# Optimization experiments

Measured on AMD Instinct MI355X. Metric: run time of the kernel, lower is better.

Reference implementation:

```python
import jax, jax.numpy as jnp
import numpy as np
from jax import lax

D_MODEL = 1024
D_STATE = 16
D_CONV = 4
EXPAND = 2
D_INNER = EXPAND * D_MODEL
DT_RANK = (D_MODEL + 15) // 16  # ceil(d_model/16) = 64


def setup_inputs() -> dict:
    key = jax.random.key(0)
    ks = jax.random.split(key, 10)
    B, L = 4, 2048
    hidden_states = jax.random.normal(ks[0], (B, L, D_MODEL), dtype=jnp.float32)
    # parameters
    in_proj_w = jax.random.normal(ks[1], (2 * D_INNER, D_MODEL), dtype=jnp.float32) / np.sqrt(D_MODEL)
    conv_w = jax.random.normal(ks[2], (D_INNER, D_CONV), dtype=jnp.float32) / np.sqrt(D_CONV)
    conv_b = jax.random.normal(ks[3], (D_INNER,), dtype=jnp.float32) * 0.02
    x_proj_w = jax.random.normal(ks[4], (DT_RANK + 2 * D_STATE, D_INNER), dtype=jnp.float32) / np.sqrt(D_INNER)
    dt_init_std = DT_RANK ** -0.5
    dt_proj_w = jax.random.uniform(ks[5], (D_INNER, DT_RANK), minval=-dt_init_std, maxval=dt_init_std, dtype=jnp.float32)
    # dt bias: inverse-softplus of log-uniform dt in [dt_min, dt_max]
    dt_min, dt_max = 1e-3, 1e-1
    dt = jnp.exp(jax.random.uniform(ks[6], (D_INNER,)) * (np.log(dt_max) - np.log(dt_min)) + np.log(dt_min))
    dt = jnp.clip(dt, 1e-4)
    dt_proj_b = dt + jnp.log(-jnp.expm1(-dt))
    A_log = jnp.log(jnp.broadcast_to(jnp.arange(1, D_STATE + 1, dtype=jnp.float32), (D_INNER, D_STATE)))
    D = jnp.ones((D_INNER,), dtype=jnp.float32)
    out_proj_w = jax.random.normal(ks[7], (D_MODEL, D_INNER), dtype=jnp.float32) / np.sqrt(D_INNER)
    return {"hidden_states": hidden_states, "in_proj_w": in_proj_w, "conv_w": conv_w,
            "conv_b": conv_b, "x_proj_w": x_proj_w, "dt_proj_w": dt_proj_w,
            "dt_proj_b": dt_proj_b, "A_log": A_log, "D": D, "out_proj_w": out_proj_w}


def reference(hidden_states, in_proj_w, conv_w, conv_b, x_proj_w, dt_proj_w, dt_proj_b, A_log, D, out_proj_w):
    Bb, L, _ = hidden_states.shape
    # input projection -> x, z each (B, L, d_inner)
    xz = jnp.einsum('bld,ed->ble', hidden_states, in_proj_w)
    x, z = jnp.split(xz, 2, axis=-1)
    # depthwise causal conv1d over time, then SiLU
    x_c = jnp.transpose(x, (0, 2, 1))  # (B, Di, L)
    x_c = lax.conv_general_dilated(x_c, conv_w[:, None, :], window_strides=(1,),
                                   padding=[(D_CONV - 1, 0)], feature_group_count=D_INNER,
                                   dimension_numbers=('NCH', 'OIH', 'NCH'))
    x_act = jax.nn.silu(x_c + conv_b[:, None])            # (B, Di, L)
    u = jnp.transpose(x_act, (0, 2, 1))                   # (B, L, Di)
    # time-variant dt, B, C projections
    x_dbl = jnp.einsum('bld,ed->ble', u, x_proj_w)        # (B, L, R+2N)
    dt_lo = x_dbl[..., :DT_RANK]
    Bm = x_dbl[..., DT_RANK:DT_RANK + D_STATE]            # (B, L, N)
    Cm = x_dbl[..., DT_RANK + D_STATE:]                   # (B, L, N)
    delta = jax.nn.softplus(jnp.einsum('blr,dr->bld', dt_lo, dt_proj_w) + dt_proj_b)  # (B, L, Di)
    A = -jnp.exp(A_log)                                   # (Di, N)

    def step(h, inp):
        d_t, b_t, c_t, u_t = inp                          # (B,Di),(B,N),(B,N),(B,Di)
        dA = jnp.exp(d_t[:, :, None] * A)                 # (B, Di, N)
        h = h * dA + (d_t * u_t)[:, :, None] * b_t[:, None, :]
        y_t = jnp.einsum('bdn,bn->bd', h, c_t)
        return h, y_t

    h0 = jnp.zeros((Bb, D_INNER, D_STATE), dtype=jnp.float32)
    xs = (jnp.swapaxes(delta, 0, 1), jnp.swapaxes(Bm, 0, 1), jnp.swapaxes(Cm, 0, 1), jnp.swapaxes(u, 0, 1))
    _, ys = lax.scan(step, h0, xs)                        # (L, B, Di)
    y = jnp.swapaxes(ys, 0, 1) + D * u                    # skip connection D*u
    y = y * jax.nn.silu(z)                                # gating
    return jnp.einsum('bld,od->blo', y, out_proj_w)
```

## Files before the change

### kernel.cpp

```cpp
#include <hip/hip_runtime.h>
#include <cmath>

#define BATCH   4
#define SEQLEN  2048
#define NTOK    (BATCH*SEQLEN)
#define DMODEL  1024
#define DINNER  2048
#define DSTATE  16
#define DTRANK  64
#define NCHUNK  32
#define LCHUNK  64

typedef unsigned short u16;
typedef __attribute__((ext_vector_type(8))) short          bf16x8;
typedef __attribute__((ext_vector_type(8))) unsigned short u16x8;
typedef __attribute__((ext_vector_type(4))) float          f32x4;

__device__ __forceinline__ float sigmoid_precise(float x){ return 1.f/(1.f+expf(-x)); }
__device__ __forceinline__ float b2f(u16 h){ return __uint_as_float(((unsigned)h)<<16); }
__device__ __forceinline__ u16 f2b(float x){
    unsigned u = __float_as_uint(x);
    u += 0x7fffu + ((u>>16)&1u);
    return (u16)(u>>16);
}
__device__ __forceinline__ ushort4 pack4(float a,float b,float c,float d){
    ushort4 r; r.x=f2b(a); r.y=f2b(b); r.z=f2b(c); r.w=f2b(d); return r;
}

__device__ __forceinline__ void gld_lds16(const void* g, void* l){
    __builtin_amdgcn_global_load_lds(
        (const __attribute__((address_space(1))) void*)g,
        (__attribute__((address_space(3))) void*)l,
        16, 0, 0);
}

__device__ __forceinline__ void decay_powers(float e1, float* dec){
    float e2=e1*e1, e3=e2*e1, e4=e2*e2;
    float e5=e4*e1, e6=e4*e2, e7=e4*e3, e8=e4*e4;
    dec[0]=e1; dec[1]=e2; dec[2]=e3; dec[3]=e4;
    dec[4]=e5; dec[5]=e6; dec[6]=e7; dec[7]=e8;
    dec[8]=e8*e1; dec[9]=e8*e2; dec[10]=e8*e3; dec[11]=e8*e4;
    dec[12]=e8*e5; dec[13]=e8*e6; dec[14]=e8*e7; dec[15]=e8*e8;
}

#define CVT_N0 (NTOK*DMODEL/8)
#define CVT_N1 (2*DINNER*DMODEL/8)
#define CVT_N2 (DMODEL*DINNER/8)
#define CVT_N3 (96*DINNER/8)
#define CVT_N4 (DINNER*DTRANK/8)
#define CVT_TOT (CVT_N0+CVT_N1+CVT_N2+CVT_N3+CVT_N4)

__global__ __launch_bounds__(256)
void cvt_all(const float* __restrict__ s0, const float* __restrict__ s1,
             const float* __restrict__ s2, const float* __restrict__ s3,
             const float* __restrict__ s4, u16* __restrict__ dst)
{
    int i = blockIdx.x*256 + threadIdx.x;
    if (i >= CVT_TOT) return;
    const float* s; int off = i;
    if      (off <  CVT_N0){ s = s0; }
    else if ((off -= CVT_N0) < CVT_N1){ s = s1; }
    else if ((off -= CVT_N1) < CVT_N2){ s = s2; }
    else if ((off -= CVT_N2) < CVT_N3){ s = s3; }
    else    { off -= CVT_N3; s = s4; }
    const float4* sp = (const float4*)(s + (size_t)off*8);
    float4 a = sp[0], b = sp[1];
    *(ushort4*)(dst + (size_t)i*8)     = pack4(a.x,a.y,a.z,a.w);
    *(ushort4*)(dst + (size_t)i*8 + 4) = pack4(b.x,b.y,b.z,b.w);
}

__global__ __launch_bounds__(512, 1)
void gemm_xz8(const u16* __restrict__ A, const u16* __restrict__ B,
              u16* __restrict__ Cx, u16* __restrict__ Cz)
{
    __shared__ u16 lds[2][2][256*64];
    const int tid  = threadIdx.x;
    const int lane = tid & 63;
    const int wave = tid >> 6;
    const int wm = wave >> 2, wn = wave & 3;
    const int fr = lane & 15, quad = lane >> 4;
    const int bid = blockIdx.x;
    const int swz = (bid & 7) * 64 + (bid >> 3);
    const int m0 = (swz >> 4) * 256;
    const int n0 = (swz & 15) * 256;
    const int NT = DMODEL / 64;

    const int srow  = tid >> 3;
    const int colsw = (((tid & 7) ^ (srow & 7)) << 3);
    const u16* gA = A + (size_t)(m0 + srow)*DMODEL + colsw;
    const u16* gB = B + (size_t)(n0 + srow)*DMODEL + colsw;

#define STAGE_A(t,h) do{ \
    const u16* g_ = gA + (size_t)((h)*128)*DMODEL + (t)*64; \
    u16* l_ = &lds[(t)&1][0][(h)*8192 + tid*8]; \
    gld_lds16(g_, l_); gld_lds16(g_ + (size_t)64*DMODEL, l_ + 4096); }while(0)
#define STAGE_B(t,h) do{ \
    const u16* g_ = gB + (size_t)((h)*128)*DMODEL + (t)*64; \
    u16* l_ = &lds[(t)&1][1][(h)*8192 + tid*8]; \
    gld_lds16(g_, l_); gld_lds16(g_ + (size_t)64*DMODEL, l_ + 4096); }while(0)

    const int cs0 = ((quad    ) ^ (fr & 7)) << 3;
    const int cs1 = ((quad + 4) ^ (fr & 7)) << 3;
    const int aoff = (wm*128 + fr) * 64;
    const int boff = (wn*64  + fr) * 64;

    f32x4 acc[8][4];
#pragma unroll
    for (int m=0;m<8;m++)
#pragma unroll
        for (int n=0;n<4;n++)
#pragma unroll
            for (int e=0;e<4;e++) acc[m][n][e] = 0.f;

    STAGE_A(0,0); STAGE_A(0,1); STAGE_B(0,0); STAGE_B(0,1);
    STAGE_B(1,0); STAGE_B(1,1);
    asm volatile("s_waitcnt vmcnt(4)" ::: "memory");
    __builtin_amdgcn_s_barrier();
    __builtin_amdgcn_sched_barrier(0);

#define XZ_MFMA_PAIR(MB) \
    _Pragma("unroll") \
    for (int n=0;n<4;n++){ \
        acc[MB][n]   = __builtin_amdgcn_mfma_f32_16x16x32_bf16(aP0, bF[n][0], acc[MB][n],   0,0,0); \
        acc[MB][n]   = __builtin_amdgcn_mfma_f32_16x16x32_bf16(aP1, bF[n][1], acc[MB][n],   0,0,0); \
        acc[MB+1][n] = __builtin_amdgcn_mfma_f32_16x16x32_bf16(aQ0, bF[n][0], acc[MB+1][n], 0,0,0); \
        acc[MB+1][n] = __builtin_amdgcn_mfma_f32_16x16x32_bf16(aQ1, bF[n][1], acc[MB+1][n], 0,0,0); \
    }

    for (int t=0; t<NT; ++t){
        const u16* lA = &lds[t&1][0][0];
        const u16* lB = &lds[t&1][1][0];
        bf16x8 bF[4][2];

        {
            bf16x8 aP0 = *(const bf16x8*)&lA[aoff + 0*1024 + cs0];
            bf16x8 aP1 = *(const bf16x8*)&lA[aoff + 0*1024 + cs1];
            bf16x8 aQ0 = *(const bf16x8*)&lA[aoff + 1*1024 + cs0];
            bf16x8 aQ1 = *(const bf16x8*)&lA[aoff + 1*1024 + cs1];
#pragma unroll
            for (int n=0;n<4;n++){
                bF[n][0] = *(const bf16x8*)&lB[boff + n*1024 + cs0];
                bF[n][1] = *(const bf16x8*)&lB[boff + n*1024 + cs1];
            }
            if (t+1 < NT) STAGE_A(t+1,0);
            asm volatile("s_waitcnt lgkmcnt(8)" ::: "memory");
            __builtin_amdgcn_s_barrier();
            asm volatile("s_waitcnt lgkmcnt(0)" ::: "memory");
            __builtin_amdgcn_s_setprio(1);
            XZ_MFMA_PAIR(0)
            __builtin_amdgcn_s_setprio(0);
            __builtin_amdgcn_s_barrier();
            __builtin_amdgcn_sched_barrier(0);
        }
        {
            bf16x8 aP0 = *(const bf16x8*)&lA[aoff + 2*1024 + cs0];
            bf16x8 aP1 = *(const bf16x8*)&lA[aoff + 2*1024 + cs1];
            bf16x8 aQ0 = *(const bf16x8*)&lA[aoff + 3*1024 + cs0];
            bf16x8 aQ1 = *(const bf16x8*)&lA[aoff + 3*1024 + cs1];
            if (t+2 < NT) STAGE_B(t+2,0);
            __builtin_amdgcn_s_barrier();
            asm volatile("s_waitcnt lgkmcnt(0)" ::: "memory");
            __builtin_amdgcn_s_setprio(1);
            XZ_MFMA_PAIR(2)
            __builtin_amdgcn_s_setprio(0);
            __builtin_amdgcn_s_barrier();
            __builtin_amdgcn_sched_barrier(0);
        }
        {
            bf16x8 aP0 = *(const bf16x8*)&lA[aoff + 4*1024 + cs0];
            bf16x8 aP1 = *(const bf16x8*)&lA[aoff + 4*1024 + cs1];
            bf16x8 aQ0 = *(const bf16x8*)&lA[aoff + 5*1024 + cs0];
            bf16x8 aQ1 = *(const bf16x8*)&lA[aoff + 5*1024 + cs1];
            if (t+1 < NT) STAGE_A(t+1,1);
            __builtin_amdgcn_s_barrier();
            asm volatile("s_waitcnt lgkmcnt(0)" ::: "memory");
            __builtin_amdgcn_s_setprio(1);
            XZ_MFMA_PAIR(4)
            __builtin_amdgcn_s_setprio(0);
            __builtin_amdgcn_s_barrier();
            __builtin_amdgcn_sched_barrier(0);
        }
        {
            bf16x8 aP0 = *(const bf16x8*)&lA[aoff + 6*1024 + cs0];
            bf16x8 aP1 = *(const bf16x8*)&lA[aoff + 6*1024 + cs1];
            bf16x8 aQ0 = *(const bf16x8*)&lA[aoff + 7*1024 + cs0];
            bf16x8 aQ1 = *(const bf16x8*)&lA[aoff + 7*1024 + cs1];
            if (t+2 < NT) STAGE_B(t+2,1);
            __builtin_amdgcn_s_barrier();
            asm volatile("s_waitcnt lgkmcnt(0)" ::: "memory");
            __builtin_amdgcn_s_setprio(1);
            XZ_MFMA_PAIR(6)
            __builtin_amdgcn_s_setprio(0);
            if (t < NT-2) asm volatile("s_waitcnt vmcnt(2)" ::: "memory");
            else          asm volatile("s_waitcnt vmcnt(0)" ::: "memory");
            __builtin_amdgcn_s_barrier();
            __builtin_amdgcn_sched_barrier(0);
        }
    }
#undef XZ_MFMA_PAIR
#undef STAGE_A
#undef STAGE_B

    const bool is_z = (n0 >= DINNER);
    u16* dst = is_z ? Cz : Cx;
    const int nb = (is_z ? n0 - DINNER : n0) + wn*64;
#pragma unroll
    for (int m=0;m<8;m++){
        const int rbase = m0 + wm*128 + m*16 + quad*4;
#pragma unroll
        for (int reg=0;reg<4;reg++){
            const int row = rbase + reg;
#pragma unroll
            for (int n=0;n<4;n++){
                float x = acc[m][n][reg];
                if (is_z) x = x * sigmoid_precise(x);
                dst[(size_t)row*DINNER + nb + n*16 + fr] = f2b(x);
            }
        }
    }
}

template<int EPI>
__global__ __launch_bounds__(256, 4)
void gemm_bt(const u16* __restrict__ A, int lda,
             const u16* __restrict__ B, int ldb,
             void* __restrict__ Cx, void* __restrict__ Cz, int ldc,
             int K)
{
    __shared__ u16 As[128*32];
    __shared__ u16 Bs[128*32];
    const int tid  = threadIdx.x;
    const int lane = tid & 63, wave = tid >> 6;
    const int wm = (wave & 1) * 64, wn = (wave >> 1) * 64;
    const int fr = lane & 15, quad = lane >> 4;
    const int m0 = blockIdx.y * 128;
    const int n0 = blockIdx.x * 128;

    f32x4 acc[4][4];
#pragma unroll
    for (int i=0;i<4;i++)
#pragma unroll
        for (int j=0;j<4;j++)
#pragma unroll
            for (int e=0;e<4;e++) acc[i][j][e] = 0.f;

    for (int k0=0;k0<K;k0+=32){
#pragma unroll
        for (int r=0;r<2;r++){
            int i = tid + 256*r;
            gld_lds16(&A[(size_t)(m0 + (i>>2))*lda + k0 + (i&3)*8], &As[(size_t)i*8]);
        }
#pragma unroll
        for (int r=0;r<2;r++){
            int i = tid + 256*r;
            gld_lds16(&B[(size_t)(n0 + (i>>2))*ldb + k0 + (i&3)*8], &Bs[(size_t)i*8]);
        }
        __syncthreads();

        bf16x8 af[4], bfg[4];
#pragma unroll
        for (int i=0;i<4;i++) af[i]  = *(const bf16x8*)&As[(wm + i*16 + fr)*32 + quad*8];
#pragma unroll
        for (int j=0;j<4;j++) bfg[j] = *(const bf16x8*)&Bs[(wn + j*16 + fr)*32 + quad*8];
#pragma unroll
        for (int i=0;i<4;i++)
#pragma unroll
            for (int j=0;j<4;j++)
                acc[i][j] = __builtin_amdgcn_mfma_f32_16x16x32_bf16(af[i], bfg[j], acc[i][j], 0,0,0);
        __syncthreads();
    }

    if (EPI==0){
        float* C = (float*)Cx;
#pragma unroll
        for (int i=0;i<4;i++){
            int rbase = m0 + wm + i*16 + quad*4;
#pragma unroll
            for (int reg=0;reg<4;reg++){
                int row = rbase + reg;
#pragma unroll
                for (int j=0;j<4;j++)
                    C[(size_t)row*ldc + n0 + wn + j*16 + fr] = acc[i][j][reg];
            }
        }
    } else {
        const bool is_z = (n0 >= DINNER);
        u16* dst = is_z ? (u16*)Cz : (u16*)Cx;
        const int nb = is_z ? (n0 - DINNER) : n0;
#pragma unroll
        for (int i=0;i<4;i++){
            int rbase = m0 + wm + i*16 + quad*4;
#pragma unroll
            for (int reg=0;reg<4;reg++){
                int row = rbase + reg;
#pragma unroll
                for (int j=0;j<4;j++){
                    float x = acc[i][j][reg];
                    if (is_z) x = x * sigmoid_precise(x);
                    dst[(size_t)row*ldc + nb + wn + j*16 + fr] = f2b(x);
                }
            }
        }
    }
}

__global__ __launch_bounds__(256)
void conv_silu_sw(const u16* __restrict__ xb, const float* __restrict__ conv_w,
                  const float* __restrict__ conv_b, u16* __restrict__ ub)
{
    const int d0 = (blockIdx.x*256 + threadIdx.x)*4;
    const int bl = blockIdx.y;
    const int b  = bl >> 6, lc = bl & 63;
    const int l0 = lc*32;
    float4 w[4]; float bias[4];
#pragma unroll
    for (int j=0;j<4;j++){ w[j] = *(const float4*)&conv_w[(d0+j)*4]; bias[j] = conv_b[d0+j]; }

    const size_t base = (size_t)b*SEQLEN*DINNER + d0;
    float win[4][3];
#pragma unroll
    for (int j=0;j<4;j++) win[j][0]=win[j][1]=win[j][2]=0.f;
    if (l0 > 0){
#pragma unroll
        for (int t=0;t<3;t++){
            ushort4 v = *(const ushort4*)&xb[base + (size_t)(l0-3+t)*DINNER];
            win[0][t]=b2f(v.x); win[1][t]=b2f(v.y); win[2][t]=b2f(v.z); win[3][t]=b2f(v.w);
        }
    }
    for (int l=l0; l<l0+32; l++){
        ushort4 v = *(const ushort4*)&xb[base + (size_t)l*DINNER];
        float x3[4] = {b2f(v.x), b2f(v.y), b2f(v.z), b2f(v.w)};
        ushort4 o;
        u16* op = (u16*)&o;
#pragma unroll
        for (int j=0;j<4;j++){
            float acc = bias[j];
            acc = fmaf(w[j].x, win[j][0], acc);
            acc = fmaf(w[j].y, win[j][1], acc);
            acc = fmaf(w[j].z, win[j][2], acc);
            acc = fmaf(w[j].w, x3[j],     acc);
            op[j] = f2b(acc * sigmoid_precise(acc));
            win[j][0]=win[j][1]; win[j][1]=win[j][2]; win[j][2]=x3[j];
        }
        *(ushort4*)&ub[base + (size_t)l*DINNER] = o;
    }
}

__global__ __launch_bounds__(256, 4)
void gemm_xproj_mfma(const u16* __restrict__ u, const u16* __restrict__ W,
                     u16* __restrict__ dtlo, float* __restrict__ bc)
{
    __shared__ u16 As[3][32*64];
    __shared__ u16 Bs[3][96*64];
    const int tid  = threadIdx.x;
    const int lane = tid & 63, wave = tid >> 6;
    const int fr = lane & 15, quad = lane >> 4;
    const int mi = wave & 1, nh = wave >> 1;
    const int m0 = blockIdx.x * 32;
    const int NT = DINNER/64;

    const int arow = (tid & 127) >> 2;
    const u16* pA = u + (size_t)(m0 + arow)*DINNER + (tid>>7)*32 + (tid&3)*8;
    const u16* pB[3];
#pragma unroll
    for (int r=0;r<3;r++){
        int i = tid + 256*r;
        int ks = (i >= 384) ? 1 : 0;
        int rem = i - ks*384;
        pB[r] = W + (size_t)(rem>>2)*DINNER + ks*32 + (rem&3)*8;
    }

#pragma unroll
    for (int t=0; t<2; ++t){
        gld_lds16(pA + t*64, &As[t][tid*8]);
#pragma unroll
        for (int r=0;r<3;r++)
            gld_lds16(pB[r] + t*64, &Bs[t][(tid + 256*r)*8]);
    }

    f32x4 acc[3];
#pragma unroll
    for (int j=0;j<3;j++)
#pragma unroll
        for (int e=0;e<4;e++) acc[j][e] = 0.f;

    int s = 0;
    for (int t=0; t<NT; ++t){
        if (t < NT-1) asm volatile("s_waitcnt vmcnt(4) lgkmcnt(0)" ::: "memory");
        else          asm volatile("s_waitcnt vmcnt(0) lgkmcnt(0)" ::: "memory");
        __builtin_amdgcn_s_barrier();

        if (t+2 < NT){
            int sn = s - 1; if (sn < 0) sn = 2;
            gld_lds16(pA + (t+2)*64, &As[sn][tid*8]);
#pragma unroll
            for (int r=0;r<3;r++)
                gld_lds16(pB[r] + (t+2)*64, &Bs[sn][(tid + 256*r)*8]);
        }

        const u16* lA = &As[s][0];
        const u16* lB = &Bs[s][0];
#pragma unroll
        for (int ks=0;ks<2;ks++){
            bf16x8 af = *(const bf16x8*)&lA[ks*(32*32) + (mi*16 + fr)*32 + quad*8];
#pragma unroll
            for (int j=0;j<3;j++){
                int nf = nh*3 + j;
                bf16x8 bf = *(const bf16x8*)&lB[ks*(96*32) + (nf*16 + fr)*32 + quad*8];
                acc[j] = __builtin_amdgcn_mfma_f32_16x16x32_bf16(af, bf, acc[j], 0,0,0);
            }
        }
        s = (s == 2) ? 0 : s + 1;
    }

#pragma unroll
    for (int j=0;j<3;j++){
        const int nf = nh*3 + j;
#pragma unroll
        for (int reg=0;reg<4;reg++){
            int row = m0 + mi*16 + quad*4 + reg;
            if (nf < 4) dtlo[(size_t)row*64 + nf*16 + fr] = f2b(acc[j][reg]);
            else        bc[(size_t)row*32 + (nf-4)*16 + fr] = acc[j][reg];
        }
    }
}

__global__ __launch_bounds__(256, 2)
void gemm_delta_mfma(const u16* __restrict__ A, const u16* __restrict__ B,
                     const float* __restrict__ bias, u16* __restrict__ delta)
{
    __shared__ u16 As[128][72];
    __shared__ u16 Bs[128][72];
    const int tid  = threadIdx.x;
    const int lane = tid & 63, wave = tid >> 6;
    const int wm = (wave & 1) * 64, wn = (wave >> 1) * 64;
    const int fr = lane & 15, quad = lane >> 4;
    const int m0 = blockIdx.y * 128;
    const int n0 = blockIdx.x * 128;

#pragma unroll
    for (int r=0;r<4;r++){
        int idx = tid + 256*r;
        int row = idx >> 3, c8 = (idx & 7)*8;
        *(u16x8*)&As[row][c8] = *(const u16x8*)&A[(size_t)(m0+row)*DTRANK + c8];
        *(u16x8*)&Bs[row][c8] = *(const u16x8*)&B[(size_t)(n0+row)*DTRANK + c8];
    }
    __syncthreads();

    f32x4 acc[4][4];
#pragma unroll
    for (int i=0;i<4;i++)
#pragma unroll
        for (int j=0;j<4;j++)
#pragma unroll
            for (int e=0;e<4;e++) acc[i][j][e] = 0.f;

#pragma unroll
    for (int ks=0;ks<2;ks++){
        bf16x8 af[4], bfg[4];
#pragma unroll
        for (int i=0;i<4;i++) af[i]  = *(const bf16x8*)&As[wm + i*16 + fr][ks*32 + quad*8];
#pragma unroll
        for (int j=0;j<4;j++) bfg[j] = *(const bf16x8*)&Bs[wn + j*16 + fr][ks*32 + quad*8];
#pragma unroll
        for (int i=0;i<4;i++)
#pragma unroll
            for (int j=0;j<4;j++)
                acc[i][j] = __builtin_amdgcn_mfma_f32_16x16x32_bf16(af[i], bfg[j], acc[i][j], 0,0,0);
    }

#pragma unroll
    for (int i=0;i<4;i++){
        int rbase = m0 + wm + i*16 + quad*4;
#pragma unroll
        for (int reg=0;reg<4;reg++){
            int row = rbase + reg;
#pragma unroll
            for (int j=0;j<4;j++){
                int col = n0 + wn + j*16 + fr;
                float x = acc[i][j][reg] + bias[col];
                float sp = (x > 20.f) ? x : log1pf(__expf(x));
                delta[(size_t)row*DINNER + col] = f2b(sp);
            }
        }
    }
}

__global__ __launch_bounds__(256)
void scan_phase1(const u16* __restrict__ delta, const u16* __restrict__ ub,
                 const float* __restrict__ bc,
                 float* __restrict__ Stot, float* __restrict__ hbuf)
{
    __shared__ float bs[LCHUNK][DSTATE];
    const int tid = threadIdx.x;
    const int d = blockIdx.x*256 + tid;
    const int c = blockIdx.y, b = blockIdx.z;
    const int l0 = c*LCHUNK;
    for (int i=tid; i<LCHUNK*DSTATE; i+=256){
        int lp = i>>4, n = i&15;
        bs[lp][n] = bc[(size_t)(b*SEQLEN + l0 + lp)*32 + n];
    }
    __syncthreads();

    float h[16];
#pragma unroll
    for (int n=0;n<16;n++) h[n]=0.f;
    float s = 0.f;
    for (int lp=0; lp<LCHUNK; lp++){
        const size_t m = (size_t)(b*SEQLEN + l0 + lp);
        const float dlt = b2f(delta[m*DINNER + d]);
        const float uu  = b2f(ub[m*DINNER + d]);
        s += dlt;
        const float du = dlt*uu;
        float dec[16];
        decay_powers(__expf(-dlt), dec);
#pragma unroll
        for (int n=0;n<16;n++)
            h[n] = fmaf(h[n], dec[n], du*bs[lp][n]);
    }
    const int bc_i = b*NCHUNK + c;
    Stot[(size_t)bc_i*DINNER + d] = s;
#pragma unroll
    for (int n=0;n<16;n++)
        hbuf[((size_t)bc_i*16 + n)*DINNER + d] = h[n];
}

__global__ __launch_bounds__(256)
void scan_phase2(const float* __restrict__ Stot, float* hbuf)
{
    const int idx = blockIdx.x*256 + threadIdx.x;
    const int d  = idx & (DINNER-1);
    const int bn = idx >> 11;
    const int n  = bn & 15;
    const int b  = bn >> 4;
    const float An = -(float)(n+1);
    float h = 0.f;
    for (int c=0;c<NCHUNK;c++){
        const int bc = b*NCHUNK + c;
        const size_t off = ((size_t)bc*16 + n)*DINNER + d;
        const float he    = hbuf[off];
        const float decay = __expf(An * Stot[(size_t)bc*DINNER + d]);
        hbuf[off] = h;
        h = fmaf(h, decay, he);
    }
}

__global__ __launch_bounds__(256)
void scan_phase3(u16* dy, const u16* __restrict__ ub, const u16* __restrict__ gz,
                 const float* __restrict__ bc,
                 const float* __restrict__ Dw, const float* __restrict__ hbuf)
{
    __shared__ float bcs[LCHUNK][32];
    const int tid = threadIdx.x;
    const int d = blockIdx.x*256 + tid;
    const int c = blockIdx.y, b = blockIdx.z;
    const int l0 = c*LCHUNK;
    for (int i=tid; i<LCHUNK*32; i+=256){
        int lp = i>>5, j = i&31;
        bcs[lp][j] = bc[(size_t)(b*SEQLEN + l0 + lp)*32 + j];
    }
    const float Dd = Dw[d];
    const int bc_i = b*NCHUNK + c;
    float h[16];
#pragma unroll
    for (int n=0;n<16;n++) h[n] = hbuf[((size_t)bc_i*16 + n)*DINNER + d];
    __syncthreads();

    for (int lp=0; lp<LCHUNK; lp++){
        const size_t m = (size_t)(b*SEQLEN + l0 + lp);
        const float dlt = b2f(dy[m*DINNER + d]);
        const float uu  = b2f(ub[m*DINNER + d]);
        const float du  = dlt*uu;
        float dec[16];
        decay_powers(__expf(-dlt), dec);
        float yv = 0.f;
#pragma unroll
        for (int n=0;n<16;n++){
            h[n] = fmaf(h[n], dec[n], du*bcs[lp][n]);
            yv   = fmaf(h[n], bcs[lp][16+n], yv);
        }
        yv = fmaf(Dd, uu, yv);
        const float g = b2f(gz[m*DINNER + d]);
        dy[m*DINNER + d] = f2b(yv * g);
    }
}

extern "C" void kernel_launch(void* const* d_in, const int* in_sizes, int n_in,
                              void* d_out, int out_size, void* d_ws, size_t ws_size,
                              hipStream_t stream)
{
    const float* hidden   = (const float*)d_in[0];
    const float* in_proj  = (const float*)d_in[1];
    const float* conv_w   = (const float*)d_in[2];
    const float* conv_b   = (const float*)d_in[3];
    const float* x_proj   = (const float*)d_in[4];
    const float* dt_proj  = (const float*)d_in[5];
    const float* dt_bias  = (const float*)d_in[6];
    const float* Dw       = (const float*)d_in[8];
    const float* out_proj = (const float*)d_in[9];
    float* out = (float*)d_out;

    u16* buf1 = (u16*)d_ws;
    u16* gz   = buf1 + (size_t)NTOK*DINNER;
    u16* ub   = gz   + (size_t)NTOK*DINNER;
    u16* dtlo = ub   + (size_t)NTOK*DINNER;
    float* bc   = (float*)(dtlo + (size_t)NTOK*64);
    float* Stot = bc   + (size_t)NTOK*32;
    float* hbuf = Stot + (size_t)BATCH*NCHUNK*DINNER;
    u16* hid_b  = (u16*)(hbuf + (size_t)BATCH*NCHUNK*DSTATE*DINNER);
    u16* win_b  = hid_b + (size_t)NTOK*DMODEL;
    u16* wout_b = win_b + (size_t)2*DINNER*DMODEL;
    u16* wx_b   = wout_b + (size_t)DMODEL*DINNER;
    u16* wdt_b  = wx_b  + (size_t)96*DINNER;
    const size_t need = ((size_t)(wdt_b - (u16*)d_ws) + (size_t)DINNER*DTRANK) * 2;
    if (ws_size < need) return;

    cvt_all<<<dim3((CVT_TOT+255)/256), 256, 0, stream>>>(
        hidden, in_proj, out_proj, x_proj, dt_proj, hid_b);

    gemm_xz8<<<dim3(512), 512, 0, stream>>>(hid_b, win_b, buf1, gz);

    conv_silu_sw<<<dim3(DINNER/1024, BATCH*64), 256, 0, stream>>>(
        buf1, conv_w, conv_b, ub);

    gemm_xproj_mfma<<<dim3(NTOK/32), 256, 0, stream>>>(ub, wx_b, dtlo, bc);

    gemm_delta_mfma<<<dim3(DINNER/128, NTOK/128), 256, 0, stream>>>(
        dtlo, wdt_b, dt_bias, buf1);

    scan_phase1<<<dim3(DINNER/256, NCHUNK, BATCH), 256, 0, stream>>>(
        buf1, ub, bc, Stot, hbuf);
    scan_phase2<<<dim3(BATCH*DSTATE*DINNER/256), 256, 0, stream>>>(Stot, hbuf);
    scan_phase3<<<dim3(DINNER/256, NCHUNK, BATCH), 256, 0, stream>>>(
        buf1, ub, gz, bc, Dw, hbuf);

    gemm_bt<0><<<dim3(DMODEL/128, NTOK/128), 256, 0, stream>>>(
        buf1, DINNER, wout_b, DINNER, out, nullptr, DMODEL, DINNER);
}
```

Baseline: 442.9 us.

## Replace output-projection GEMM with pipelined 256x128 tile kernel and reorder xz staging

The output projection previously used a simple 128x128 GEMM with a 32-wide K step and synchronous LDS staging. It is replaced by a 512-thread kernel with 256x128 tiles, 64-wide K steps, double-buffered XOR-swizzled LDS, async global-to-LDS prefetch, block swizzling and MFMA priority hints, mirroring the existing xz GEMM. The xz GEMM also reorders when A and B are staged within an iteration and relaxes its vmcnt wait. The new output kernel launches 256 blocks at one block per CU, which may leave part of the GPU idle, and the vmcnt change has to stay consistent with the staging order to avoid reading stale LDS.

```diff
diff --git a/kernel.cpp b/kernel.cpp
--- a/kernel.cpp
+++ b/kernel.cpp
@@ -69,6 +69,15 @@
     *(ushort4*)(dst + (size_t)i*8 + 4) = pack4(b.x,b.y,b.z,b.w);
 }
 
+#define MFMA_PAIR16(MB) \
+    _Pragma("unroll") \
+    for (int n=0;n<4;n++){ \
+        acc[MB][n]   = __builtin_amdgcn_mfma_f32_16x16x32_bf16(aP0, bF[n][0], acc[MB][n],   0,0,0); \
+        acc[MB][n]   = __builtin_amdgcn_mfma_f32_16x16x32_bf16(aP1, bF[n][1], acc[MB][n],   0,0,0); \
+        acc[MB+1][n] = __builtin_amdgcn_mfma_f32_16x16x32_bf16(aQ0, bF[n][0], acc[MB+1][n], 0,0,0); \
+        acc[MB+1][n] = __builtin_amdgcn_mfma_f32_16x16x32_bf16(aQ1, bF[n][1], acc[MB+1][n], 0,0,0); \
+    }
+
 __global__ __launch_bounds__(512, 1)
 void gemm_xz8(const u16* __restrict__ A, const u16* __restrict__ B,
               u16* __restrict__ Cx, u16* __restrict__ Cz)
@@ -118,15 +127,6 @@
     __builtin_amdgcn_s_barrier();
     __builtin_amdgcn_sched_barrier(0);
 
-#define XZ_MFMA_PAIR(MB) \
-    _Pragma("unroll") \
-    for (int n=0;n<4;n++){ \
-        acc[MB][n]   = __builtin_amdgcn_mfma_f32_16x16x32_bf16(aP0, bF[n][0], acc[MB][n],   0,0,0); \
-        acc[MB][n]   = __builtin_amdgcn_mfma_f32_16x16x32_bf16(aP1, bF[n][1], acc[MB][n],   0,0,0); \
-        acc[MB+1][n] = __builtin_amdgcn_mfma_f32_16x16x32_bf16(aQ0, bF[n][0], acc[MB+1][n], 0,0,0); \
-        acc[MB+1][n] = __builtin_amdgcn_mfma_f32_16x16x32_bf16(aQ1, bF[n][1], acc[MB+1][n], 0,0,0); \
-    }
-
     for (int t=0; t<NT; ++t){
         const u16* lA = &lds[t&1][0][0];
         const u16* lB = &lds[t&1][1][0];
@@ -147,7 +147,7 @@
             __builtin_amdgcn_s_barrier();
             asm volatile("s_waitcnt lgkmcnt(0)" ::: "memory");
             __builtin_amdgcn_s_setprio(1);
-            XZ_MFMA_PAIR(0)
+            MFMA_PAIR16(0)
             __builtin_amdgcn_s_setprio(0);
             __builtin_amdgcn_s_barrier();
             __builtin_amdgcn_sched_barrier(0);
@@ -157,11 +157,11 @@
             bf16x8 aP1 = *(const bf16x8*)&lA[aoff + 2*1024 + cs1];
             bf16x8 aQ0 = *(const bf16x8*)&lA[aoff + 3*1024 + cs0];
             bf16x8 aQ1 = *(const bf16x8*)&lA[aoff + 3*1024 + cs1];
-            if (t+2 < NT) STAGE_B(t+2,0);
+            if (t+1 < NT) STAGE_A(t+1,1);
             __builtin_amdgcn_s_barrier();
             asm volatile("s_waitcnt lgkmcnt(0)" ::: "memory");
             __builtin_amdgcn_s_setprio(1);
-            XZ_MFMA_PAIR(2)
+            MFMA_PAIR16(2)
             __builtin_amdgcn_s_setprio(0);
             __builtin_amdgcn_s_barrier();
             __builtin_amdgcn_sched_barrier(0);
@@ -171,11 +171,11 @@
             bf16x8 aP1 = *(const bf16x8*)&lA[aoff + 4*1024 + cs1];
             bf16x8 aQ0 = *(const bf16x8*)&lA[aoff + 5*1024 + cs0];
             bf16x8 aQ1 = *(const bf16x8*)&lA[aoff + 5*1024 + cs1];
-            if (t+1 < NT) STAGE_A(t+1,1);
+            if (t+2 < NT) STAGE_B(t+2,0);
             __builtin_amdgcn_s_barrier();
             asm volatile("s_waitcnt lgkmcnt(0)" ::: "memory");
             __builtin_amdgcn_s_setprio(1);
-            XZ_MFMA_PAIR(4)
+            MFMA_PAIR16(4)
             __builtin_amdgcn_s_setprio(0);
             __builtin_amdgcn_s_barrier();
             __builtin_amdgcn_sched_barrier(0);
@@ -189,15 +189,14 @@
             __builtin_amdgcn_s_barrier();
             asm volatile("s_waitcnt lgkmcnt(0)" ::: "memory");
             __builtin_amdgcn_s_setprio(1);
-            XZ_MFMA_PAIR(6)
+            MFMA_PAIR16(6)
             __builtin_amdgcn_s_setprio(0);
-            if (t < NT-2) asm volatile("s_waitcnt vmcnt(2)" ::: "memory");
+            if (t < NT-2) asm volatile("s_waitcnt vmcnt(4)" ::: "memory");
             else          asm volatile("s_waitcnt vmcnt(0)" ::: "memory");
             __builtin_amdgcn_s_barrier();
             __builtin_amdgcn_sched_barrier(0);
         }
     }
-#undef XZ_MFMA_PAIR
 #undef STAGE_A
 #undef STAGE_B
 
@@ -220,86 +219,113 @@
     }
 }
 
-template<int EPI>
-__global__ __launch_bounds__(256, 4)
-void gemm_bt(const u16* __restrict__ A, int lda,
-             const u16* __restrict__ B, int ldb,
-             void* __restrict__ Cx, void* __restrict__ Cz, int ldc,
-             int K)
-{
-    __shared__ u16 As[128*32];
-    __shared__ u16 Bs[128*32];
+__global__ __launch_bounds__(512, 1)
+void gemm_out8(const u16* __restrict__ A, const u16* __restrict__ B,
+               float* __restrict__ C)
+{
+    __shared__ u16 ldsA[2][256*64];
+    __shared__ u16 ldsB[2][128*64];
     const int tid  = threadIdx.x;
-    const int lane = tid & 63, wave = tid >> 6;
-    const int wm = (wave & 1) * 64, wn = (wave >> 1) * 64;
+    const int lane = tid & 63;
+    const int wave = tid >> 6;
+    const int wm = wave >> 1, wn = wave & 1;
     const int fr = lane & 15, quad = lane >> 4;
-    const int m0 = blockIdx.y * 128;
-    const int n0 = blockIdx.x * 128;
+    const int bid = blockIdx.x;
+    const int swz = (bid & 7) * 32 + (bid >> 3);
+    const int m0 = (swz >> 3) * 256;
+    const int n0 = (swz & 7) * 128;
+    const int NT = DINNER / 64;
+
+    const int srow  = tid >> 3;
+    const int colsw = (((tid & 7) ^ (srow & 7)) << 3);
+    const u16* gA = A + (size_t)(m0 + srow)*DINNER + colsw;
+    const u16* gB = B + (size_t)(n0 + srow)*DINNER + colsw;
+
+#define OSTAGE_A(t) do{ \
+    const u16* g_ = gA + (t)*64; \
+    u16* l_ = &ldsA[(t)&1][tid*8]; \
+    gld_lds16(g_,                      l_); \
+    gld_lds16(g_ + (size_t) 64*DINNER, l_ + 4096); \
+    gld_lds16(g_ + (size_t)128*DINNER, l_ + 8192); \
+    gld_lds16(g_ + (size_t)192*DINNER, l_ + 12288); }while(0)
+#define OSTAGE_B(t) do{ \
+    const u16* g_ = gB + (t)*64; \
+    u16* l_ = &ldsB[(t)&1][tid*8]; \
+    gld_lds16(g_,                      l_); \
+    gld_lds16(g_ + (size_t) 64*DINNER, l_ + 4096); }while(0)
+
+    const int cs0 = ((quad    ) ^ (fr & 7)) << 3;
+    const int cs1 = ((quad + 4) ^ (fr & 7)) << 3;
+    const int aoff = (wm*64 + fr) * 64;
+    const int boff = (wn*64 + fr) * 64;
 
     f32x4 acc[4][4];
 #pragma unroll
-    for (int i=0;i<4;i++)
-#pragma unroll
-        for (int j=0;j<4;j++)
-#pragma unroll
-            for (int e=0;e<4;e++) acc[i][j][e] = 0.f;
-
-    for (int k0=0;k0<K;k0+=32){
-#pragma unroll
-        for (int r=0;r<2;r++){
-            int i = tid + 256*r;
-            gld_lds16(&A[(size_t)(m0 + (i>>2))*lda + k0 + (i&3)*8], &As[(size_t)i*8]);
-        }
-#pragma unroll
-        for (int r=0;r<2;r++){
-            int i = tid + 256*r;
-            gld_lds16(&B[(size_t)(n0 + (i>>2))*ldb + k0 + (i&3)*8], &Bs[(size_t)i*8]);
-        }
-        __syncthreads();
-
-        bf16x8 af[4], bfg[4];
-#pragma unroll
-        for (int i=0;i<4;i++) af[i]  = *(const bf16x8*)&As[(wm + i*16 + fr)*32 + quad*8];
-#pragma unroll
-        for (int j=0;j<4;j++) bfg[j] = *(const bf16x8*)&Bs[(wn + j*16 + fr)*32 + quad*8];
-#pragma unroll
-        for (int i=0;i<4;i++)
-#pragma unroll
-            for (int j=0;j<4;j++)
-                acc[i][j] = __builtin_amdgcn_mfma_f32_16x16x32_bf16(af[i], bfg[j], acc[i][j], 0,0,0);
-        __syncthreads();
-    }
-
-    if (EPI==0){
-        float* C = (float*)Cx;
-#pragma unroll
-        for (int i=0;i<4;i++){
-            int rbase = m0 + wm + i*16 + quad*4;
-#pragma unroll
-            for (int reg=0;reg<4;reg++){
-                int row = rbase + reg;
-#pragma unroll
-                for (int j=0;j<4;j++)
-                    C[(size_t)row*ldc + n0 + wn + j*16 + fr] = acc[i][j][reg];
+    for (int m=0;m<4;m++)
+#pragma unroll
+        for (int n=0;n<4;n++)
+#pragma unroll
+            for (int e=0;e<4;e++) acc[m][n][e] = 0.f;
+
+    OSTAGE_A(0); OSTAGE_B(0); OSTAGE_B(1);
+    asm volatile("s_waitcnt vmcnt(2)" ::: "memory");
+    __builtin_amdgcn_s_barrier();
+    __builtin_amdgcn_sched_barrier(0);
+
+    for (int t=0; t<NT; ++t){
+        const u16* lA = &ldsA[t&1][0];
+        const u16* lB = &ldsB[t&1][0];
+        bf16x8 bF[4][2];
+
+        {
+            bf16x8 aP0 = *(const bf16x8*)&lA[aoff + 0*1024 + cs0];
+            bf16x8 aP1 = *(const bf16x8*)&lA[aoff + 0*1024 + cs1];
+            bf16x8 aQ0 = *(const bf16x8*)&lA[aoff + 1*1024 + cs0];
+            bf16x8 aQ1 = *(const bf16x8*)&lA[aoff + 1*1024 + cs1];
+#pragma unroll
+            for (int n=0;n<4;n++){
+                bF[n][0] = *(const bf16x8*)&lB[boff + n*1024 + cs0];
+                bF[n][1] = *(const bf16x8*)&lB[boff + n*1024 + cs1];
             }
-        }
-    } else {
-        const bool is_z = (n0 >= DINNER);
-        u16* dst = is_z ? (u16*)Cz : (u16*)Cx;
-        const int nb = is_z ? (n0 - DINNER) : n0;
-#pragma unroll
-        for (int i=0;i<4;i++){
-            int rbase = m0 + wm + i*16 + quad*4;
-#pragma unroll
-            for (int reg=0;reg<4;reg++){
-                int row = rbase + reg;
-#pragma unroll
-                for (int j=0;j<4;j++){
-                    float x = acc[i][j][reg];
-                    if (is_z) x = x * sigmoid_precise(x);
-                    dst[(size_t)row*ldc + nb + wn + j*16 + fr] = f2b(x);
-                }
-            }
+            if (t+1 < NT) OSTAGE_A(t+1);
+            asm volatile("s_waitcnt lgkmcnt(8)" ::: "memory");
+            __builtin_amdgcn_s_barrier();
+            asm volatile("s_waitcnt lgkmcnt(0)" ::: "memory");
+            __builtin_amdgcn_s_setprio(1);
+            MFMA_PAIR16(0)
+            __builtin_amdgcn_s_setprio(0);
+            __builtin_amdgcn_s_barrier();
+            __builtin_amdgcn_sched_barrier(0);
+        }
+        {
+            bf16x8 aP0 = *(const bf16x8*)&lA[aoff + 2*1024 + cs0];
+            bf16x8 aP1 = *(const bf16x8*)&lA[aoff + 2*1024 + cs1];
+            bf16x8 aQ0 = *(const bf16x8*)&lA[aoff + 3*1024 + cs0];
+            bf16x8 aQ1 = *(const bf16x8*)&lA[aoff + 3*1024 + cs1];
+            if (t+2 < NT) OSTAGE_B(t+2);
+            __builtin_amdgcn_s_barrier();
+            asm volatile("s_waitcnt lgkmcnt(0)" ::: "memory");
+            __builtin_amdgcn_s_setprio(1);
+            MFMA_PAIR16(2)
+            __builtin_amdgcn_s_setprio(0);
+            if (t < NT-2) asm volatile("s_waitcnt vmcnt(2)" ::: "memory");
+            else          asm volatile("s_waitcnt vmcnt(0)" ::: "memory");
+            __builtin_amdgcn_s_barrier();
+            __builtin_amdgcn_sched_barrier(0);
+        }
+    }
+#undef OSTAGE_A
+#undef OSTAGE_B
+
+#pragma unroll
+    for (int m=0;m<4;m++){
+        const int rbase = m0 + wm*64 + m*16 + quad*4;
+#pragma unroll
+        for (int reg=0;reg<4;reg++){
+            const int row = rbase + reg;
+#pragma unroll
+            for (int n=0;n<4;n++)
+                C[(size_t)row*DMODEL + n0 + wn*64 + n*16 + fr] = acc[m][n][reg];
         }
     }
 }
@@ -634,6 +660,5 @@
     scan_phase3<<<dim3(DINNER/256, NCHUNK, BATCH), 256, 0, stream>>>(
         buf1, ub, gz, bc, Dw, hbuf);
 
-    gemm_bt<0><<<dim3(DMODEL/128, NTOK/128), 256, 0, stream>>>(
-        buf1, DINNER, wout_b, DINNER, out, nullptr, DMODEL, DINNER);
-}
+    gemm_out8<<<dim3(256), 512, 0, stream>>>(buf1, wout_b, out);
+}
```

Result: faster. 431.3 us (-2.6%).
